# Kernel tuning notes

Hardware: AMD Instinct MI355X
Metric: run time of the kernel (lower is better)

The kernel has to match this reference:

```python
import jax, jax.numpy as jnp
import numpy as np

N_NODES = 50000
N_EDGES = 800000
C_IN = 128
C_OUT = 64
C_HID = 2 * C_OUT  # 128


def setup_inputs() -> dict:
    key = jax.random.key(0)
    ks = jax.random.split(key, 8)
    x = jax.random.normal(ks[0], (N_NODES, C_IN), dtype=jnp.float32)
    edge_index = jax.random.randint(ks[1], (2, N_EDGES), 0, N_NODES, dtype=jnp.int64)
    s1 = 1.0 / np.sqrt(C_IN)
    s2 = 1.0 / np.sqrt(C_HID)
    s3 = 1.0 / np.sqrt(C_OUT)
    W1 = jax.random.uniform(ks[2], (C_IN, C_HID), jnp.float32, -s1, s1)
    b1 = jnp.zeros((C_HID,), jnp.float32)
    W2 = jax.random.uniform(ks[3], (C_HID, C_OUT), jnp.float32, -s2, s2)
    b2 = jnp.zeros((C_OUT,), jnp.float32)
    Wb = jax.random.uniform(ks[4], (1, C_OUT, C_OUT), jnp.float32, -s3, s3)
    bb = jax.random.uniform(ks[5], (1,), jnp.float32, -s3, s3)
    return {"x": x, "edge_index": edge_index, "W1": W1, "b1": b1,
            "W2": W2, "b2": b2, "Wb": Wb, "bb": bb}


def gcn_conv(x, W, b, src, dst, n_nodes):
    # PyG GCNConv: h = x @ W; add self-loops; symmetric normalization D^-1/2 (A+I) D^-1/2.
    h = x @ W  # [N, F]
    ones = jnp.ones((src.shape[0],), h.dtype)
    deg = jax.ops.segment_sum(ones, dst, num_segments=n_nodes) + 1.0  # +1 for self-loop
    dinv = jax.lax.rsqrt(deg)
    norm = dinv[src] * dinv[dst]  # [E]
    msgs = h[src] * norm[:, None]  # [E, F]
    agg = jax.ops.segment_sum(msgs, dst, num_segments=n_nodes)
    # self-loop contribution: norm_ii = 1/deg_i
    agg = agg + h * (1.0 / deg)[:, None]
    return agg + b


def reference(x, edge_index, W1, b1, W2, b2, Wb, bb):
    src = edge_index[0]
    dst = edge_index[1]
    n = x.shape[0]
    # encode
    h = jax.nn.relu(gcn_conv(x, W1, b1, src, dst, n))
    z = gcn_conv(h, W2, b2, src, dst, n)  # [N, C_OUT]
    # decode: bilinear on (z[src], z[dst]) -> sigmoid
    zs = z[src]  # [E, C_OUT]
    zd = z[dst]  # [E, C_OUT]
    logits = jnp.einsum('ec,ocd,ed->eo', zs, Wb, zd) + bb  # [E, 1]
    return jax.nn.sigmoid(logits)
```

## Files before the change

### kernel.cpp

```cpp
#include <hip/hip_runtime.h>
#include <hip/hip_bf16.h>


#define N_NODES 50000
#define BSH 7
#define BSZ 128
#define NBUCK ((N_NODES + BSZ - 1) / BSZ)
#define EPB 4096
#define CAP 3072
#define DSPLIT 8

typedef unsigned int u32;
typedef unsigned short u16;
typedef unsigned long long u64;

typedef __attribute__((ext_vector_type(8))) short bf16x8;
typedef __attribute__((ext_vector_type(4))) float f32x4;
union frag_u { bf16x8 f; u32 u[4]; uint4 v; };

__device__ __forceinline__ float bflo(u32 u) { return __uint_as_float(u << 16); }
__device__ __forceinline__ float bfhi(u32 u) { return __uint_as_float(u & 0xffff0000u); }
__device__ __forceinline__ u32 f2bf(float f) {
    u32 b = __float_as_uint(f);
    return (b + 0x7fffu + ((b >> 16) & 1u)) >> 16;
}
__device__ __forceinline__ u32 pack2(float a, float b) { return f2bf(a) | (f2bf(b) << 16); }

__global__ __launch_bounds__(256) void gemm1_scatter(
        const float* __restrict__ X, const float* __restrict__ W,
        u16* __restrict__ O, int n_rows, int gblk,
        const int* __restrict__ src, const int* __restrict__ dst,
        int* __restrict__ bcur, u64* __restrict__ pair, int E) {
    constexpr int K = 128, NOUT = 128;
    constexpr int KP = K + 8;
    constexpr int NT = NOUT / 16;
    constexpr int KS = K / 32;
    __shared__ __align__(16) char smem[NOUT * KP * 2 * sizeof(u16)];
    int t = threadIdx.x;

    if ((int)blockIdx.x < gblk) {
        u16* Wt_hi = (u16*)smem;
        u16* Wt_lo = Wt_hi + NOUT * KP;
        for (int i4 = t; i4 < K * NOUT / 4; i4 += 256) {
            int k = (i4 * 4) / NOUT;
            int n0 = (i4 * 4) % NOUT;
            float4 w4 = *(const float4*)&W[(size_t)k * NOUT + n0];
            float wv[4] = {w4.x, w4.y, w4.z, w4.w};
#pragma unroll
            for (int q = 0; q < 4; q++) {
                u32 hi = f2bf(wv[q]);
                u32 lo = f2bf(wv[q] - bflo(hi));
                Wt_hi[(n0 + q) * KP + k] = (u16)hi;
                Wt_lo[(n0 + q) * KP + k] = (u16)lo;
            }
        }
        __syncthreads();

        int wave = t >> 6;
        int lane = t & 63;
        int m16 = lane & 15;
        int quad = lane >> 4;
        int row0 = blockIdx.x * 128 + wave * 32;

        f32x4 acc[2][NT] = {};
        for (int ks = 0; ks < KS; ks++) {
            frag_u a_hi[2], a_lo[2];
#pragma unroll
            for (int mt = 0; mt < 2; mt++) {
                int row = row0 + mt * 16 + m16;
                row = row < n_rows ? row : n_rows - 1;
                const float* Xp = X + (size_t)row * K + ks * 32 + quad * 8;
                float4 x0 = *(const float4*)Xp;
                float4 x1 = *(const float4*)(Xp + 4);
                float xv[8] = {x0.x, x0.y, x0.z, x0.w, x1.x, x1.y, x1.z, x1.w};
#pragma unroll
                for (int p = 0; p < 4; p++) {
                    u32 h0 = f2bf(xv[2 * p]), h1 = f2bf(xv[2 * p + 1]);
                    a_hi[mt].u[p] = h0 | (h1 << 16);
                    a_lo[mt].u[p] = pack2(xv[2 * p] - bflo(h0), xv[2 * p + 1] - bflo(h1));
                }
            }
#pragma unroll
            for (int nt = 0; nt < NT; nt++) {
                int n = nt * 16 + m16;
                frag_u b_hi, b_lo;
                b_hi.v = *(const uint4*)&Wt_hi[n * KP + ks * 32 + quad * 8];
                b_lo.v = *(const uint4*)&Wt_lo[n * KP + ks * 32 + quad * 8];
#pragma unroll
                for (int mt = 0; mt < 2; mt++) {
                    acc[mt][nt] = __builtin_amdgcn_mfma_f32_16x16x32_bf16(a_hi[mt].f, b_hi.f, acc[mt][nt], 0, 0, 0);
                    acc[mt][nt] = __builtin_amdgcn_mfma_f32_16x16x32_bf16(a_hi[mt].f, b_lo.f, acc[mt][nt], 0, 0, 0);
                    acc[mt][nt] = __builtin_amdgcn_mfma_f32_16x16x32_bf16(a_lo[mt].f, b_hi.f, acc[mt][nt], 0, 0, 0);
                }
            }
        }
#pragma unroll
        for (int mt = 0; mt < 2; mt++)
#pragma unroll
            for (int nt = 0; nt < NT; nt++)
#pragma unroll
                for (int r = 0; r < 4; r++) {
                    int row = row0 + mt * 16 + quad * 4 + r;
                    if (row < n_rows)
                        O[(size_t)row * NOUT + nt * 16 + m16] = (u16)f2bf(acc[mt][nt][r]);
                }
    } else {
        int* hist = (int*)smem;
        for (int i = t; i < NBUCK; i += 256) hist[i] = 0;
        __syncthreads();
        int base = ((int)blockIdx.x - gblk) * EPB;
        int s_[16], d_[16];
#pragma unroll
        for (int it = 0; it < 16; it++) {
            int e = base + it * 256 + t;
            if (e < E) {
                s_[it] = src[e];
                d_[it] = dst[e];
                atomicAdd(&hist[d_[it] >> BSH], 1);
            } else {
                d_[it] = -1;
            }
        }
        __syncthreads();
        for (int b = t; b < NBUCK; b += 256) {
            int c = hist[b];
            hist[b] = c ? (b * CAP + atomicAdd(&bcur[b], c)) : 0;
        }
        __syncthreads();
#pragma unroll
        for (int it = 0; it < 16; it++) {
            if (d_[it] >= 0) {
                int b = d_[it] >> BSH;
                int off = atomicAdd(&hist[b], 1);
                int e = base + it * 256 + t;
                pair[off] = (u64)((u32)s_[it] | ((u32)(d_[it] & (BSZ - 1)) << 16))
                          | ((u64)(u32)e << 32);
            }
        }
    }
}

__global__ __launch_bounds__(256) void bucket_sort(u64* __restrict__ pair,
                                                   const int* __restrict__ bcur,
                                                   int* __restrict__ row_ptr,
                                                   int* __restrict__ col,
                                                   float* __restrict__ dinv,
                                                   float* __restrict__ inv, int n, int E) {
    __shared__ u64 prA[CAP];
    __shared__ u64 prB[CAP];
    __shared__ int ssum[256];
    __shared__ int histA[512];
    __shared__ int scA[512];
    __shared__ int cnt[BSZ];
    __shared__ int scn[BSZ];
    __shared__ int cur[BSZ];
    int t = threadIdx.x;
    int bucket = blockIdx.x;
    int base = bucket << BSH;
    int nn = min(BSZ, n - base);
    int accp = 0;
    for (int i = t; i < bucket; i += 256) accp += bcur[i];
    ssum[t] = accp;
    __syncthreads();
    for (int s = 128; s > 0; s >>= 1) {
        if (t < s) ssum[t] += ssum[t + s];
        __syncthreads();
    }
    int b0 = ssum[0];
    int cntE = bcur[bucket];
    int p0 = bucket * CAP;

    histA[t] = 0;
    histA[t + 256] = 0;
    __syncthreads();
    for (int j = t; j < cntE; j += 256) {
        u64 p = pair[p0 + j];
        prA[j] = p;
        atomicAdd(&histA[(int)(p & 0xffffu) >> BSH], 1);
    }
    __syncthreads();
    int h0 = histA[t], h1 = histA[t + 256];
    scA[t] = h0;
    scA[t + 256] = h1;
    __syncthreads();
    for (int off = 1; off < 512; off <<= 1) {
        int a0 = (t >= off) ? scA[t - off] : 0;
        int a1 = (t + 256 >= off) ? scA[t + 256 - off] : 0;
        __syncthreads();
        scA[t] += a0;
        scA[t + 256] += a1;
        __syncthreads();
    }
    histA[t] = scA[t] - h0;
    histA[t + 256] = scA[t + 256] - h1;
    __syncthreads();
    for (int j = t; j < cntE; j += 256) {
        u64 p = prA[j];
        int pos = atomicAdd(&histA[(int)(p & 0xffffu) >> BSH], 1);
        prB[pos] = p;
    }
    __syncthreads();
    for (int j = t; j < cntE; j += 256) pair[p0 + j] = prB[j];

    if (t < BSZ) cnt[t] = 0;
    __syncthreads();
    for (int j = t; j < cntE; j += 256)
        atomicAdd(&cnt[(int)((prB[j] >> 16) & (BSZ - 1))], 1);
    __syncthreads();
    if (t < BSZ) scn[t] = cnt[t];
    __syncthreads();
    for (int off = 1; off < BSZ; off <<= 1) {
        int a = (t < BSZ && t >= off) ? scn[t - off] : 0;
        __syncthreads();
        if (t < BSZ) scn[t] += a;
        __syncthreads();
    }
    if (t < nn) {
        int excl = b0 + scn[t] - cnt[t];
        row_ptr[base + t] = excl;
        cur[t] = excl;
        float d = (float)cnt[t] + 1.0f;
        dinv[base + t] = rsqrtf(d);
        inv[base + t] = 1.0f / d;
    }
    if (t == 0 && bucket == NBUCK - 1) row_ptr[n] = E;
    __syncthreads();
    for (int j = t; j < cntE; j += 256) {
        u64 p = prB[j];
        int ln = (int)((p >> 16) & (BSZ - 1));
        int pos = atomicAdd(&cur[ln], 1);
        col[pos] = (int)(p & 0xffffu);
    }
}

template <int K, int NOUT>
__global__ __launch_bounds__(256) void gemm_mfma_bf(const u16* __restrict__ Xv,
                                                    const float* __restrict__ W,
                                                    u16* __restrict__ O, int n_rows) {
    constexpr int KP = K + 8;
    constexpr int NT = NOUT / 16;
    constexpr int KS = K / 32;
    __shared__ __align__(16) u16 Wt_hi[NOUT * KP];
    __shared__ __align__(16) u16 Wt_lo[NOUT * KP];
    int t = threadIdx.x;
    for (int i4 = t; i4 < K * NOUT / 4; i4 += 256) {
        int k = (i4 * 4) / NOUT;
        int n0 = (i4 * 4) % NOUT;
        float4 w4 = *(const float4*)&W[(size_t)k * NOUT + n0];
        float wv[4] = {w4.x, w4.y, w4.z, w4.w};
#pragma unroll
        for (int q = 0; q < 4; q++) {
            u32 hi = f2bf(wv[q]);
            u32 lo = f2bf(wv[q] - bflo(hi));
            Wt_hi[(n0 + q) * KP + k] = (u16)hi;
            Wt_lo[(n0 + q) * KP + k] = (u16)lo;
        }
    }
    __syncthreads();

    int wave = t >> 6;
    int lane = t & 63;
    int m16 = lane & 15;
    int quad = lane >> 4;
    int row0 = blockIdx.x * 128 + wave * 32;

    f32x4 acc[2][NT] = {};
    for (int ks = 0; ks < KS; ks++) {
        frag_u a_hi[2];
#pragma unroll
        for (int mt = 0; mt < 2; mt++) {
            int row = row0 + mt * 16 + m16;
            row = row < n_rows ? row : n_rows - 1;
            a_hi[mt].v = *(const uint4*)(Xv + (size_t)row * K + ks * 32 + quad * 8);
        }
#pragma unroll
        for (int nt = 0; nt < NT; nt++) {
            int n = nt * 16 + m16;
            frag_u b_hi, b_lo;
            b_hi.v = *(const uint4*)&Wt_hi[n * KP + ks * 32 + quad * 8];
            b_lo.v = *(const uint4*)&Wt_lo[n * KP + ks * 32 + quad * 8];
#pragma unroll
            for (int mt = 0; mt < 2; mt++) {
                acc[mt][nt] = __builtin_amdgcn_mfma_f32_16x16x32_bf16(a_hi[mt].f, b_hi.f, acc[mt][nt], 0, 0, 0);
                acc[mt][nt] = __builtin_amdgcn_mfma_f32_16x16x32_bf16(a_hi[mt].f, b_lo.f, acc[mt][nt], 0, 0, 0);
            }
        }
    }
#pragma unroll
    for (int mt = 0; mt < 2; mt++)
#pragma unroll
        for (int nt = 0; nt < NT; nt++)
#pragma unroll
            for (int r = 0; r < 4; r++) {
                int row = row0 + mt * 16 + quad * 4 + r;
                if (row < n_rows)
                    O[(size_t)row * NOUT + nt * 16 + m16] = (u16)f2bf(acc[mt][nt][r]);
            }
}

#define ACC4(va, vb, vc, vd, na, nb, nc, nd)                                          \
    acc[0] += bflo(va.x) * na + bflo(vb.x) * nb + bflo(vc.x) * nc + bflo(vd.x) * nd;  \
    acc[1] += bfhi(va.x) * na + bfhi(vb.x) * nb + bfhi(vc.x) * nc + bfhi(vd.x) * nd;  \
    acc[2] += bflo(va.y) * na + bflo(vb.y) * nb + bflo(vc.y) * nc + bflo(vd.y) * nd;  \
    acc[3] += bfhi(va.y) * na + bfhi(vb.y) * nb + bfhi(vc.y) * nc + bfhi(vd.y) * nd;  \
    acc[4] += bflo(va.z) * na + bflo(vb.z) * nb + bflo(vc.z) * nc + bflo(vd.z) * nd;  \
    acc[5] += bfhi(va.z) * na + bfhi(vb.z) * nb + bfhi(vc.z) * nc + bfhi(vd.z) * nd;  \
    acc[6] += bflo(va.w) * na + bflo(vb.w) * nb + bflo(vc.w) * nc + bflo(vd.w) * nd;  \
    acc[7] += bfhi(va.w) * na + bfhi(vb.w) * nb + bfhi(vc.w) * nc + bfhi(vd.w) * nd;

template <int C, bool RELU>
__global__ __launch_bounds__(256) void agg_pull(const u16* __restrict__ H,
                                                const int* __restrict__ row_ptr,
                                                const int* __restrict__ col,
                                                const float* __restrict__ dinv,
                                                const float* __restrict__ inv,
                                                const float* __restrict__ b,
                                                u16* __restrict__ O, int n) {
    constexpr int TPN = C / 8;
    const uint4* Hv = (const uint4*)H;
    int tid = blockIdx.x * 256 + threadIdx.x;
    int node = tid / TPN;
    if (node >= n) return;
    int part = tid % TPN;
    int c8 = part * 8;
    float dn = dinv[node];
    float iv = inv[node];
    float acc[8];
    {
        uint4 h = Hv[(size_t)node * TPN + part];
        acc[0] = bflo(h.x) * iv + b[c8 + 0];
        acc[1] = bfhi(h.x) * iv + b[c8 + 1];
        acc[2] = bflo(h.y) * iv + b[c8 + 2];
        acc[3] = bfhi(h.y) * iv + b[c8 + 3];
        acc[4] = bflo(h.z) * iv + b[c8 + 4];
        acc[5] = bfhi(h.z) * iv + b[c8 + 5];
        acc[6] = bflo(h.w) * iv + b[c8 + 6];
        acc[7] = bfhi(h.w) * iv + b[c8 + 7];
    }
    int j = row_ptr[node];
    int end = row_ptr[node + 1];
    for (; j + 15 < end; j += 16) {
        int s0 = col[j],      s1 = col[j + 1],  s2 = col[j + 2],  s3 = col[j + 3];
        int s4 = col[j + 4],  s5 = col[j + 5],  s6 = col[j + 6],  s7 = col[j + 7];
        int s8 = col[j + 8],  s9 = col[j + 9],  sa = col[j + 10], sb = col[j + 11];
        int sc = col[j + 12], sd = col[j + 13], se = col[j + 14], sf = col[j + 15];
        float n0 = dn * dinv[s0], n1 = dn * dinv[s1], n2 = dn * dinv[s2], n3 = dn * dinv[s3];
        float n4 = dn * dinv[s4], n5 = dn * dinv[s5], n6 = dn * dinv[s6], n7 = dn * dinv[s7];
        float n8 = dn * dinv[s8], n9 = dn * dinv[s9], na = dn * dinv[sa], nb = dn * dinv[sb];
        float nc = dn * dinv[sc], nd = dn * dinv[sd], ne = dn * dinv[se], nf = dn * dinv[sf];
        uint4 v0 = Hv[(size_t)s0 * TPN + part];
        uint4 v1 = Hv[(size_t)s1 * TPN + part];
        uint4 v2 = Hv[(size_t)s2 * TPN + part];
        uint4 v3 = Hv[(size_t)s3 * TPN + part];
        uint4 v4 = Hv[(size_t)s4 * TPN + part];
        uint4 v5 = Hv[(size_t)s5 * TPN + part];
        uint4 v6 = Hv[(size_t)s6 * TPN + part];
        uint4 v7 = Hv[(size_t)s7 * TPN + part];
        uint4 v8 = Hv[(size_t)s8 * TPN + part];
        uint4 v9 = Hv[(size_t)s9 * TPN + part];
        uint4 va = Hv[(size_t)sa * TPN + part];
        uint4 vb = Hv[(size_t)sb * TPN + part];
        uint4 vc = Hv[(size_t)sc * TPN + part];
        uint4 vd = Hv[(size_t)sd * TPN + part];
        uint4 ve = Hv[(size_t)se * TPN + part];
        uint4 vf = Hv[(size_t)sf * TPN + part];
        ACC4(v0, v1, v2, v3, n0, n1, n2, n3)
        ACC4(v4, v5, v6, v7, n4, n5, n6, n7)
        ACC4(v8, v9, va, vb, n8, n9, na, nb)
        ACC4(vc, vd, ve, vf, nc, nd, ne, nf)
    }
    for (; j + 7 < end; j += 8) {
        int s0 = col[j],     s1 = col[j + 1], s2 = col[j + 2], s3 = col[j + 3];
        int s4 = col[j + 4], s5 = col[j + 5], s6 = col[j + 6], s7 = col[j + 7];
        float n0 = dn * dinv[s0], n1 = dn * dinv[s1], n2 = dn * dinv[s2], n3 = dn * dinv[s3];
        float n4 = dn * dinv[s4], n5 = dn * dinv[s5], n6 = dn * dinv[s6], n7 = dn * dinv[s7];
        uint4 v0 = Hv[(size_t)s0 * TPN + part];
        uint4 v1 = Hv[(size_t)s1 * TPN + part];
        uint4 v2 = Hv[(size_t)s2 * TPN + part];
        uint4 v3 = Hv[(size_t)s3 * TPN + part];
        uint4 v4 = Hv[(size_t)s4 * TPN + part];
        uint4 v5 = Hv[(size_t)s5 * TPN + part];
        uint4 v6 = Hv[(size_t)s6 * TPN + part];
        uint4 v7 = Hv[(size_t)s7 * TPN + part];
        ACC4(v0, v1, v2, v3, n0, n1, n2, n3)
        ACC4(v4, v5, v6, v7, n4, n5, n6, n7)
    }
    for (; j + 3 < end; j += 4) {
        int s0 = col[j], s1 = col[j + 1], s2 = col[j + 2], s3 = col[j + 3];
        float n0 = dn * dinv[s0], n1 = dn * dinv[s1], n2 = dn * dinv[s2], n3 = dn * dinv[s3];
        uint4 v0 = Hv[(size_t)s0 * TPN + part];
        uint4 v1 = Hv[(size_t)s1 * TPN + part];
        uint4 v2 = Hv[(size_t)s2 * TPN + part];
        uint4 v3 = Hv[(size_t)s3 * TPN + part];
        ACC4(v0, v1, v2, v3, n0, n1, n2, n3)
    }
    for (; j < end; j++) {
        int s = col[j];
        float nm = dn * dinv[s];
        uint4 v = Hv[(size_t)s * TPN + part];
        acc[0] += bflo(v.x) * nm; acc[1] += bfhi(v.x) * nm;
        acc[2] += bflo(v.y) * nm; acc[3] += bfhi(v.y) * nm;
        acc[4] += bflo(v.z) * nm; acc[5] += bfhi(v.z) * nm;
        acc[6] += bflo(v.w) * nm; acc[7] += bfhi(v.w) * nm;
    }
    if (RELU) {
#pragma unroll
        for (int i = 0; i < 8; i++) acc[i] = fmaxf(acc[i], 0.f);
    }
    uint4 o;
    o.x = pack2(acc[0], acc[1]);
    o.y = pack2(acc[2], acc[3]);
    o.z = pack2(acc[4], acc[5]);
    o.w = pack2(acc[6], acc[7]);
    ((uint4*)O)[(size_t)node * TPN + part] = o;
}

__global__ __launch_bounds__(256) void decode_fused(const u16* __restrict__ Z,
                                                    const float* __restrict__ Wb,
                                                    const u64* __restrict__ pair,
                                                    const int* __restrict__ bcur,
                                                    const float* __restrict__ bb,
                                                    float* __restrict__ out, int n) {
    constexpr int K = 64, NOUT = 64;
    constexpr int KP = K + 8;
    constexpr int QP = 72;
    __shared__ __align__(16) u16 Wt_hi[NOUT * KP];
    __shared__ __align__(16) u16 Wt_lo[NOUT * KP];
    __shared__ __align__(16) u16 Qs[BSZ * QP];
    int t = threadIdx.x;
    int bucket = blockIdx.x / DSPLIT;
    int part = blockIdx.x % DSPLIT;
    int base = bucket << BSH;

    for (int i4 = t; i4 < K * NOUT / 4; i4 += 256) {
        int nn_ = (i4 * 4) / K;
        int k0 = (i4 * 4) % K;
        float4 w4 = *(const float4*)&Wb[(size_t)nn_ * K + k0];
        float wv[4] = {w4.x, w4.y, w4.z, w4.w};
#pragma unroll
        for (int q = 0; q < 4; q++) {
            u32 hi = f2bf(wv[q]);
            u32 lo = f2bf(wv[q] - bflo(hi));
            Wt_hi[nn_ * KP + k0 + q] = (u16)hi;
            Wt_lo[nn_ * KP + k0 + q] = (u16)lo;
        }
    }
    __syncthreads();

    {
        int wave = t >> 6;
        int lane = t & 63;
        int m16 = lane & 15;
        int quad = lane >> 4;
        int row0 = wave * 32;
        f32x4 acc[2][4] = {};
        for (int ks = 0; ks < 2; ks++) {
            frag_u a[2];
#pragma unroll
            for (int mt = 0; mt < 2; mt++) {
                int node = base + row0 + mt * 16 + m16;
                node = node < n ? node : n - 1;
                a[mt].v = *(const uint4*)(Z + (size_t)node * K + ks * 32 + quad * 8);
            }
#pragma unroll
            for (int nt = 0; nt < 4; nt++) {
                int nc = nt * 16 + m16;
                frag_u b_hi, b_lo;
                b_hi.v = *(const uint4*)&Wt_hi[nc * KP + ks * 32 + quad * 8];
                b_lo.v = *(const uint4*)&Wt_lo[nc * KP + ks * 32 + quad * 8];
#pragma unroll
                for (int mt = 0; mt < 2; mt++) {
                    acc[mt][nt] = __builtin_amdgcn_mfma_f32_16x16x32_bf16(a[mt].f, b_hi.f, acc[mt][nt], 0, 0, 0);
                    acc[mt][nt] = __builtin_amdgcn_mfma_f32_16x16x32_bf16(a[mt].f, b_lo.f, acc[mt][nt], 0, 0, 0);
                }
            }
        }
#pragma unroll
        for (int mt = 0; mt < 2; mt++)
#pragma unroll
            for (int nt = 0; nt < 4; nt++)
#pragma unroll
                for (int r = 0; r < 4; r++) {
                    int rl = row0 + mt * 16 + quad * 4 + r;
                    Qs[rl * QP + nt * 16 + m16] = (u16)f2bf(acc[mt][nt][r]);
                }
    }
    __syncthreads();

    const uint4* Zv = (const uint4*)Z;
    int cntE = bcur[bucket];
    int p0 = bucket * CAP;
    int chunk = (cntE + DSPLIT - 1) / DSPLIT;
    int s0 = part * chunk;
    int s1 = min(s0 + chunk, cntE);
    float bbv = bb[0];
    int lane8 = t & 7;
    int grp = t >> 3;
    for (int j = s0 + grp * 2; j < s1; j += 64) {
        u64 pA = pair[p0 + j];
        bool has2 = (j + 1) < s1;
        u64 pB = has2 ? pair[p0 + j + 1] : pA;
        int sA = (int)(pA & 0xffffu);
        int sB = (int)(pB & 0xffffu);
        int locA = (int)((pA >> 16) & (BSZ - 1));
        int locB = (int)((pB >> 16) & (BSZ - 1));
        uint4 zA = Zv[(size_t)sA * 8 + lane8];
        uint4 zB = Zv[(size_t)sB * 8 + lane8];
        uint4 qA = *(const uint4*)&Qs[locA * QP + lane8 * 8];
        uint4 qB = *(const uint4*)&Qs[locB * QP + lane8 * 8];
        float dA = bflo(zA.x) * bflo(qA.x) + bfhi(zA.x) * bfhi(qA.x)
                 + bflo(zA.y) * bflo(qA.y) + bfhi(zA.y) * bfhi(qA.y)
                 + bflo(zA.z) * bflo(qA.z) + bfhi(zA.z) * bfhi(qA.z)
                 + bflo(zA.w) * bflo(qA.w) + bfhi(zA.w) * bfhi(qA.w);
        float dB = bflo(zB.x) * bflo(qB.x) + bfhi(zB.x) * bfhi(qB.x)
                 + bflo(zB.y) * bflo(qB.y) + bfhi(zB.y) * bfhi(qB.y)
                 + bflo(zB.z) * bflo(qB.z) + bfhi(zB.z) * bfhi(qB.z)
                 + bflo(zB.w) * bflo(qB.w) + bfhi(zB.w) * bfhi(qB.w);
        dA += __shfl_down(dA, 4, 8);
        dA += __shfl_down(dA, 2, 8);
        dA += __shfl_down(dA, 1, 8);
        dB += __shfl_down(dB, 4, 8);
        dB += __shfl_down(dB, 2, 8);
        dB += __shfl_down(dB, 1, 8);
        if (lane8 == 0) {
            out[(int)(pA >> 32)] = 1.0f / (1.0f + expf(-(dA + bbv)));
            if (has2) out[(int)(pB >> 32)] = 1.0f / (1.0f + expf(-(dB + bbv)));
        }
    }
}

extern "C" void kernel_launch(void* const* d_in, const int* in_sizes, int n_in,
                              void* d_out, int out_size, void* d_ws, size_t ws_size,
                              hipStream_t stream) {
    const float* x  = (const float*)d_in[0];
    const int*   ei = (const int*)d_in[1];
    const float* W1 = (const float*)d_in[2];
    const float* b1 = (const float*)d_in[3];
    const float* W2 = (const float*)d_in[4];
    const float* b2 = (const float*)d_in[5];
    const float* Wb = (const float*)d_in[6];
    const float* bb = (const float*)d_in[7];
    float* out = (float*)d_out;

    const int N = N_NODES;
    const int E = in_sizes[1] / 2;
    const int* src = ei;
    const int* dst = ei + E;
    const int GBLK = (N + 127) / 128;
    const int SBLK = (E + EPB - 1) / EPB;

    char* w = (char*)d_ws;
    int*   bcur    = (int*)w;   w += (size_t)512 * 4;
    int*   row_ptr = (int*)w;   w += (size_t)(N + 1) * 4;
    int*   col     = (int*)w;   w += (size_t)E * 4;
    w = (char*)(((size_t)w + 15) & ~(size_t)15);
    u64*   pair    = (u64*)w;   w += (size_t)NBUCK * CAP * 8;
    float* dinv    = (float*)w; w += (size_t)N * 4;
    float* inv     = (float*)w; w += (size_t)N * 4;
    w = (char*)(((size_t)w + 15) & ~(size_t)15);
    u16* bufA = (u16*)w;        w += (size_t)N * 128 * 2;
    u16* bufB = (u16*)w;        w += (size_t)N * 128 * 2;
    u16* bufC = (u16*)w;

    u16* H1 = bufA;
    u16* h1 = bufB;
    u16* H2 = bufA;
    u16* Z  = bufC;

    hipMemsetAsync(bcur, 0, 512 * 4, stream);
    gemm1_scatter<<<GBLK + SBLK, 256, 0, stream>>>(x, W1, H1, N, GBLK,
                                                   src, dst, bcur, pair, E);
    bucket_sort<<<NBUCK, 256, 0, stream>>>(pair, bcur, row_ptr, col, dinv, inv, N, E);

    agg_pull<128, true><<<((size_t)N * 16 + 255) / 256, 256, 0, stream>>>(
        H1, row_ptr, col, dinv, inv, b1, h1, N);

    gemm_mfma_bf<128, 64><<<GBLK, 256, 0, stream>>>(h1, W2, H2, N);
    agg_pull<64, false><<<((size_t)N * 8 + 255) / 256, 256, 0, stream>>>(
        H2, row_ptr, col, dinv, inv, b2, Z, N);

    decode_fused<<<NBUCK * DSPLIT, 256, 0, stream>>>(Z, Wb, pair, bcur, bb, out, N);
}
```

Measured before the change: 239.9 us.

## Fuse layer-1 aggregation with layer-2 GEMM and trim gather unrolling

Replaces the separate layer-1 aggregation kernel and the MFMA GEMM for W2 with one kernel. Each block aggregates 16 nodes into shared memory, applies ReLU, and immediately multiplies the tile by W2 with MFMA. This removes the write and re-read of the intermediate hidden features and one launch. The cost is that every block reloads W2 from global memory and splits it into hi/lo bf16 parts itself. The change also drops the 16-wide gather unroll in agg_pull and halves DSPLIT for the decode kernel. The fused kernel has no node<n bound check, which is safe only because N is a multiple of 16.

```diff
diff --git a/kernel.cpp b/kernel.cpp
--- a/kernel.cpp
+++ b/kernel.cpp
@@ -8,7 +8,7 @@
 #define NBUCK ((N_NODES + BSZ - 1) / BSZ)
 #define EPB 4096
 #define CAP 3072
-#define DSPLIT 8
+#define DSPLIT 4
 
 typedef unsigned int u32;
 typedef unsigned short u16;
@@ -233,71 +233,6 @@
     }
 }
 
-template <int K, int NOUT>
-__global__ __launch_bounds__(256) void gemm_mfma_bf(const u16* __restrict__ Xv,
-                                                    const float* __restrict__ W,
-                                                    u16* __restrict__ O, int n_rows) {
-    constexpr int KP = K + 8;
-    constexpr int NT = NOUT / 16;
-    constexpr int KS = K / 32;
-    __shared__ __align__(16) u16 Wt_hi[NOUT * KP];
-    __shared__ __align__(16) u16 Wt_lo[NOUT * KP];
-    int t = threadIdx.x;
-    for (int i4 = t; i4 < K * NOUT / 4; i4 += 256) {
-        int k = (i4 * 4) / NOUT;
-        int n0 = (i4 * 4) % NOUT;
-        float4 w4 = *(const float4*)&W[(size_t)k * NOUT + n0];
-        float wv[4] = {w4.x, w4.y, w4.z, w4.w};
-#pragma unroll
-        for (int q = 0; q < 4; q++) {
-            u32 hi = f2bf(wv[q]);
-            u32 lo = f2bf(wv[q] - bflo(hi));
-            Wt_hi[(n0 + q) * KP + k] = (u16)hi;
-            Wt_lo[(n0 + q) * KP + k] = (u16)lo;
-        }
-    }
-    __syncthreads();
-
-    int wave = t >> 6;
-    int lane = t & 63;
-    int m16 = lane & 15;
-    int quad = lane >> 4;
-    int row0 = blockIdx.x * 128 + wave * 32;
-
-    f32x4 acc[2][NT] = {};
-    for (int ks = 0; ks < KS; ks++) {
-        frag_u a_hi[2];
-#pragma unroll
-        for (int mt = 0; mt < 2; mt++) {
-            int row = row0 + mt * 16 + m16;
-            row = row < n_rows ? row : n_rows - 1;
-            a_hi[mt].v = *(const uint4*)(Xv + (size_t)row * K + ks * 32 + quad * 8);
-        }
-#pragma unroll
-        for (int nt = 0; nt < NT; nt++) {
-            int n = nt * 16 + m16;
-            frag_u b_hi, b_lo;
-            b_hi.v = *(const uint4*)&Wt_hi[n * KP + ks * 32 + quad * 8];
-            b_lo.v = *(const uint4*)&Wt_lo[n * KP + ks * 32 + quad * 8];
-#pragma unroll
-            for (int mt = 0; mt < 2; mt++) {
-                acc[mt][nt] = __builtin_amdgcn_mfma_f32_16x16x32_bf16(a_hi[mt].f, b_hi.f, acc[mt][nt], 0, 0, 0);
-                acc[mt][nt] = __builtin_amdgcn_mfma_f32_16x16x32_bf16(a_hi[mt].f, b_lo.f, acc[mt][nt], 0, 0, 0);
-            }
-        }
-    }
-#pragma unroll
-    for (int mt = 0; mt < 2; mt++)
-#pragma unroll
-        for (int nt = 0; nt < NT; nt++)
-#pragma unroll
-            for (int r = 0; r < 4; r++) {
-                int row = row0 + mt * 16 + quad * 4 + r;
-                if (row < n_rows)
-                    O[(size_t)row * NOUT + nt * 16 + m16] = (u16)f2bf(acc[mt][nt][r]);
-            }
-}
-
 #define ACC4(va, vb, vc, vd, na, nb, nc, nd)                                          \
     acc[0] += bflo(va.x) * na + bflo(vb.x) * nb + bflo(vc.x) * nc + bflo(vd.x) * nd;  \
     acc[1] += bfhi(va.x) * na + bfhi(vb.x) * nb + bfhi(vc.x) * nc + bfhi(vd.x) * nd;  \
@@ -307,6 +242,114 @@
     acc[5] += bfhi(va.z) * na + bfhi(vb.z) * nb + bfhi(vc.z) * nc + bfhi(vd.z) * nd;  \
     acc[6] += bflo(va.w) * na + bflo(vb.w) * nb + bflo(vc.w) * nc + bflo(vd.w) * nd;  \
     acc[7] += bfhi(va.w) * na + bfhi(vb.w) * nb + bfhi(vc.w) * nc + bfhi(vd.w) * nd;
+
+__global__ __launch_bounds__(256) void agg1_gemm2(const u16* __restrict__ H,
+                                                  const int* __restrict__ row_ptr,
+                                                  const int* __restrict__ col,
+                                                  const float* __restrict__ dinv,
+                                                  const float* __restrict__ inv,
+                                                  const float* __restrict__ b,
+                                                  const float* __restrict__ W2,
+                                                  u16* __restrict__ H2, int n) {
+    constexpr int TPN = 16;
+    __shared__ __align__(16) u16 h1s[16][136];
+    const uint4* Hv = (const uint4*)H;
+    int t = threadIdx.x;
+    int tid = blockIdx.x * 256 + t;
+    int node = tid / TPN;
+    int part = tid % TPN;
+    int c8 = part * 8;
+    float dn = dinv[node];
+    float iv = inv[node];
+    float acc[8];
+    {
+        uint4 h = Hv[(size_t)node * TPN + part];
+        acc[0] = bflo(h.x) * iv + b[c8 + 0];
+        acc[1] = bfhi(h.x) * iv + b[c8 + 1];
+        acc[2] = bflo(h.y) * iv + b[c8 + 2];
+        acc[3] = bfhi(h.y) * iv + b[c8 + 3];
+        acc[4] = bflo(h.z) * iv + b[c8 + 4];
+        acc[5] = bfhi(h.z) * iv + b[c8 + 5];
+        acc[6] = bflo(h.w) * iv + b[c8 + 6];
+        acc[7] = bfhi(h.w) * iv + b[c8 + 7];
+    }
+    int j = row_ptr[node];
+    int end = row_ptr[node + 1];
+    for (; j + 7 < end; j += 8) {
+        int s0 = col[j],     s1 = col[j + 1], s2 = col[j + 2], s3 = col[j + 3];
+        int s4 = col[j + 4], s5 = col[j + 5], s6 = col[j + 6], s7 = col[j + 7];
+        float n0 = dn * dinv[s0], n1 = dn * dinv[s1], n2 = dn * dinv[s2], n3 = dn * dinv[s3];
+        float n4 = dn * dinv[s4], n5 = dn * dinv[s5], n6 = dn * dinv[s6], n7 = dn * dinv[s7];
+        uint4 v0 = Hv[(size_t)s0 * TPN + part];
+        uint4 v1 = Hv[(size_t)s1 * TPN + part];
+        uint4 v2 = Hv[(size_t)s2 * TPN + part];
+        uint4 v3 = Hv[(size_t)s3 * TPN + part];
+        uint4 v4 = Hv[(size_t)s4 * TPN + part];
+        uint4 v5 = Hv[(size_t)s5 * TPN + part];
+        uint4 v6 = Hv[(size_t)s6 * TPN + part];
+        uint4 v7 = Hv[(size_t)s7 * TPN + part];
+        ACC4(v0, v1, v2, v3, n0, n1, n2, n3)
+        ACC4(v4, v5, v6, v7, n4, n5, n6, n7)
+    }
+    for (; j + 3 < end; j += 4) {
+        int s0 = col[j], s1 = col[j + 1], s2 = col[j + 2], s3 = col[j + 3];
+        float n0 = dn * dinv[s0], n1 = dn * dinv[s1], n2 = dn * dinv[s2], n3 = dn * dinv[s3];
+        uint4 v0 = Hv[(size_t)s0 * TPN + part];
+        uint4 v1 = Hv[(size_t)s1 * TPN + part];
+        uint4 v2 = Hv[(size_t)s2 * TPN + part];
+        uint4 v3 = Hv[(size_t)s3 * TPN + part];
+        ACC4(v0, v1, v2, v3, n0, n1, n2, n3)
+    }
+    for (; j < end; j++) {
+        int s = col[j];
+        float nm = dn * dinv[s];
+        uint4 v = Hv[(size_t)s * TPN + part];
+        acc[0] += bflo(v.x) * nm; acc[1] += bfhi(v.x) * nm;
+        acc[2] += bflo(v.y) * nm; acc[3] += bfhi(v.y) * nm;
+        acc[4] += bflo(v.z) * nm; acc[5] += bfhi(v.z) * nm;
+        acc[6] += bflo(v.w) * nm; acc[7] += bfhi(v.w) * nm;
+    }
+#pragma unroll
+    for (int i = 0; i < 8; i++) acc[i] = fmaxf(acc[i], 0.f);
+    uint4 o;
+    o.x = pack2(acc[0], acc[1]);
+    o.y = pack2(acc[2], acc[3]);
+    o.z = pack2(acc[4], acc[5]);
+    o.w = pack2(acc[6], acc[7]);
+    *(uint4*)&h1s[t >> 4][c8] = o;
+    __syncthreads();
+
+    int wave = t >> 6;
+    int lane = t & 63;
+    int m16 = lane & 15;
+    int quad = lane >> 4;
+    int ncol = wave * 16 + m16;
+    f32x4 acc2 = {};
+#pragma unroll
+    for (int ks = 0; ks < 4; ks++) {
+        frag_u a, bh, bl;
+        a.v = *(const uint4*)&h1s[m16][ks * 32 + quad * 8];
+        const float* Wp = W2 + (size_t)(ks * 32 + quad * 8) * 64 + ncol;
+        float w0 = Wp[0 * 64], w1 = Wp[1 * 64], w2 = Wp[2 * 64], w3 = Wp[3 * 64];
+        float w4 = Wp[4 * 64], w5 = Wp[5 * 64], w6 = Wp[6 * 64], w7 = Wp[7 * 64];
+        u32 h0 = f2bf(w0), h1 = f2bf(w1), h2 = f2bf(w2), h3 = f2bf(w3);
+        u32 h4 = f2bf(w4), h5 = f2bf(w5), h6 = f2bf(w6), h7 = f2bf(w7);
+        bh.u[0] = h0 | (h1 << 16);
+        bh.u[1] = h2 | (h3 << 16);
+        bh.u[2] = h4 | (h5 << 16);
+        bh.u[3] = h6 | (h7 << 16);
+        bl.u[0] = pack2(w0 - bflo(h0), w1 - bflo(h1));
+        bl.u[1] = pack2(w2 - bflo(h2), w3 - bflo(h3));
+        bl.u[2] = pack2(w4 - bflo(h4), w5 - bflo(h5));
+        bl.u[3] = pack2(w6 - bflo(h6), w7 - bflo(h7));
+        acc2 = __builtin_amdgcn_mfma_f32_16x16x32_bf16(a.f, bh.f, acc2, 0, 0, 0);
+        acc2 = __builtin_amdgcn_mfma_f32_16x16x32_bf16(a.f, bl.f, acc2, 0, 0, 0);
+    }
+    int rowbase = blockIdx.x * 16 + quad * 4;
+#pragma unroll
+    for (int r = 0; r < 4; r++)
+        H2[(size_t)(rowbase + r) * 64 + ncol] = (u16)f2bf(acc2[r]);
+}
 
 template <int C, bool RELU>
 __global__ __launch_bounds__(256) void agg_pull(const u16* __restrict__ H,
@@ -339,36 +382,6 @@
     }
     int j = row_ptr[node];
     int end = row_ptr[node + 1];
-    for (; j + 15 < end; j += 16) {
-        int s0 = col[j],      s1 = col[j + 1],  s2 = col[j + 2],  s3 = col[j + 3];
-        int s4 = col[j + 4],  s5 = col[j + 5],  s6 = col[j + 6],  s7 = col[j + 7];
-        int s8 = col[j + 8],  s9 = col[j + 9],  sa = col[j + 10], sb = col[j + 11];
-        int sc = col[j + 12], sd = col[j + 13], se = col[j + 14], sf = col[j + 15];
-        float n0 = dn * dinv[s0], n1 = dn * dinv[s1], n2 = dn * dinv[s2], n3 = dn * dinv[s3];
-        float n4 = dn * dinv[s4], n5 = dn * dinv[s5], n6 = dn * dinv[s6], n7 = dn * dinv[s7];
-        float n8 = dn * dinv[s8], n9 = dn * dinv[s9], na = dn * dinv[sa], nb = dn * dinv[sb];
-        float nc = dn * dinv[sc], nd = dn * dinv[sd], ne = dn * dinv[se], nf = dn * dinv[sf];
-        uint4 v0 = Hv[(size_t)s0 * TPN + part];
-        uint4 v1 = Hv[(size_t)s1 * TPN + part];
-        uint4 v2 = Hv[(size_t)s2 * TPN + part];
-        uint4 v3 = Hv[(size_t)s3 * TPN + part];
-        uint4 v4 = Hv[(size_t)s4 * TPN + part];
-        uint4 v5 = Hv[(size_t)s5 * TPN + part];
-        uint4 v6 = Hv[(size_t)s6 * TPN + part];
-        uint4 v7 = Hv[(size_t)s7 * TPN + part];
-        uint4 v8 = Hv[(size_t)s8 * TPN + part];
-        uint4 v9 = Hv[(size_t)s9 * TPN + part];
-        uint4 va = Hv[(size_t)sa * TPN + part];
-        uint4 vb = Hv[(size_t)sb * TPN + part];
-        uint4 vc = Hv[(size_t)sc * TPN + part];
-        uint4 vd = Hv[(size_t)sd * TPN + part];
-        uint4 ve = Hv[(size_t)se * TPN + part];
-        uint4 vf = Hv[(size_t)sf * TPN + part];
-        ACC4(v0, v1, v2, v3, n0, n1, n2, n3)
-        ACC4(v4, v5, v6, v7, n4, n5, n6, n7)
-        ACC4(v8, v9, va, vb, n8, n9, na, nb)
-        ACC4(vc, vd, ve, vf, nc, nd, ne, nf)
-    }
     for (; j + 7 < end; j += 8) {
         int s0 = col[j],     s1 = col[j + 1], s2 = col[j + 2], s3 = col[j + 3];
         int s4 = col[j + 4], s5 = col[j + 5], s6 = col[j + 6], s7 = col[j + 7];
@@ -563,8 +576,7 @@
     u16* bufC = (u16*)w;
 
     u16* H1 = bufA;
-    u16* h1 = bufB;
-    u16* H2 = bufA;
+    u16* H2 = bufB;
     u16* Z  = bufC;
 
     hipMemsetAsync(bcur, 0, 512 * 4, stream);
@@ -572,10 +584,9 @@
                                                    src, dst, bcur, pair, E);
     bucket_sort<<<NBUCK, 256, 0, stream>>>(pair, bcur, row_ptr, col, dinv, inv, N, E);
 
-    agg_pull<128, true><<<((size_t)N * 16 + 255) / 256, 256, 0, stream>>>(
-        H1, row_ptr, col, dinv, inv, b1, h1, N);
-
-    gemm_mfma_bf<128, 64><<<GBLK, 256, 0, stream>>>(h1, W2, H2, N);
+    agg1_gemm2<<<((size_t)N * 16 + 255) / 256, 256, 0, stream>>>(
+        H1, row_ptr, col, dinv, inv, b1, W2, H2, N);
+
     agg_pull<64, false><<<((size_t)N * 8 + 255) / 256, 256, 0, stream>>>(
         H2, row_ptr, col, dinv, inv, b2, Z, N);
 
```

Measured after the change: 219.2 us, median of 2. 1.09x faster.
